# Kernel tuning notes

Measured on AMD Instinct MI355X. Metric: run time of the kernel, lower is better.

The kernel has to match this reference:

```python
import jax, jax.numpy as jnp
import numpy as np

EPS = 1e-6                                   # VN leaky-relu denominator eps
BN_SCALE = np.float32(1.0 / np.sqrt(1.0 + 1e-5))  # eval-mode BatchNorm with default stats
NEG = 0.2                                    # negative_slope


def vn_lin(x, w):
    # x: [n, c, 3, ...]; w: [c, o] -> [n, o, 3, ...]
    return jnp.einsum('nc...,co->no...', x, w)


def vn_act(p, d):
    # Vector-Neuron leaky ReLU: project p off the half-space defined by direction d.
    dot = jnp.sum(p * d, axis=2, keepdims=True)
    dsq = jnp.sum(d * d, axis=2, keepdims=True)
    corr = p - (dot / (dsq + EPS)) * d
    return NEG * p + (1.0 - NEG) * jnp.where(dot >= 0, p, corr)


def score_net(x, w_vn, wd_vn, w_h1, w_h2, b_h2, temp=1.0):
    # CorrelationNet: VNLinearLeakyReLU(3 -> 2*ks) -> norm -> 1x1 convs -> softmax
    p = vn_lin(x, w_vn) * BN_SCALE           # [N, 2ks, 3, K] (VNBatchNorm ~ scalar in eval)
    d = vn_lin(x, wd_vn)
    s = vn_act(p, d)
    s = jnp.linalg.norm(s, axis=2)           # [N, 2ks, K]
    s = jax.nn.relu(jnp.einsum('nck,co->nok', s, w_h1) * BN_SCALE)  # conv1d k=1, BN, relu
    s = jnp.einsum('nck,co->nok', s, w_h2) + b_h2[None, :, None]     # last conv with bias
    return jax.nn.softmax(s / temp, axis=1)  # [N, ks, K]


def setup_inputs() -> dict:
    key = jax.random.key(0)
    k = [jax.random.fold_in(key, i) for i in range(13)]
    N, N2, K, KS, OUT = 16000, 20000, 16, 8, 64
    half = OUT // 2
    return {
        'q_pts': jax.random.normal(k[0], (N, 3), jnp.float32),
        's_pts': jax.random.normal(k[1], (N2, 3), jnp.float32),
        's_feats': jax.random.normal(k[2], (N2, 1, 3), jnp.float32),
        'neighbor_indices': jax.random.randint(k[3], (N, K), 0, N2),
        'wb': jax.random.normal(k[4], (3, KS * half), jnp.float32) * np.float32(np.sqrt(2.0 / 3.0)),
        'w_vn': jax.random.normal(k[5], (3, 2 * KS), jnp.float32) * 0.5,
        'wd_vn': jax.random.normal(k[6], (3, 2 * KS), jnp.float32) * 0.5,
        'w_h1': jax.random.normal(k[7], (2 * KS, KS), jnp.float32) * 0.25,
        'w_h2': jax.random.normal(k[8], (KS, KS), jnp.float32) * 0.35,
        'b_h2': jnp.zeros((KS,), jnp.float32),
        'wd_relu': jax.random.normal(k[9], (half, half), jnp.float32) * 0.18,
        'w_un': jax.random.normal(k[10], (half, OUT), jnp.float32) * 0.18,
        'wd_un': jax.random.normal(k[11], (half, OUT), jnp.float32) * 0.18,
    }


def reference(q_pts, s_pts, s_feats, neighbor_indices, wb, w_vn, wd_vn,
              w_h1, w_h2, b_h2, wd_relu, w_un, wd_un):
    N, K = neighbor_indices.shape
    KS = w_h2.shape[1]
    # neighbor gather + centering: [N, K, 3] -> [N, 1, 3, K]
    pts = s_pts[neighbor_indices] - q_pts[:, None]
    pts = jnp.transpose(pts, (0, 2, 1))[:, None]
    centers = jnp.broadcast_to(jnp.mean(pts, axis=-1, keepdims=True), pts.shape)
    cross = jnp.cross(pts, centers, axis=2)
    local = jnp.concatenate([pts, centers, cross], axis=1)   # [N, 3, 3, K]
    scores = score_net(local, w_vn, wd_vn, w_h1, w_h2, b_h2)  # [N, KS, K]
    # kernel-point correlation conv
    pro = jnp.einsum('ncdk,cf->nfdk', local, wb)              # [N, KS*half, 3, K]
    pro = pro.reshape(N, KS, -1, 3, K)
    pro = jnp.sum(pro * scores[:, :, None, None, :], axis=1)  # [N, half, 3, K]
    nrm = jnp.linalg.norm(pro, axis=2, keepdims=True)
    normed = pro / jnp.maximum(nrm, 1e-12)                    # F.normalize(p=2, dim=2)
    feats = jnp.mean(normed, axis=-1)                         # [N, half, 3]
    feats = vn_act(feats, vn_lin(feats, wd_relu))             # VNLeakyReLU
    out = vn_act(vn_lin(feats, w_un) * BN_SCALE, vn_lin(feats, wd_un))  # VNLinearLeakyReLU
    return out                                                # [N, out_dim, 3]
```

## Files before the change

kernel.cpp:

```cpp
#include <hip/hip_runtime.h>
#include <math.h>

#define VN_EPS   1e-6f
#define NEG      0.2f
#define POS      0.8f

typedef float v2f __attribute__((ext_vector_type(2)));
typedef float v4f __attribute__((ext_vector_type(4)));

template <int CTRL>
__device__ __forceinline__ float dpp_add(float v) {
    int s = __builtin_amdgcn_update_dpp(0, __float_as_int(v), CTRL, 0xf, 0xf, true);
    return v + __int_as_float(s);
}
__device__ __forceinline__ float row16_allsum(float v) {
    v = dpp_add<0x128>(v);
    v = dpp_add<0x124>(v);
    v = dpp_add<0x122>(v);
    v = dpp_add<0x121>(v);
    return v;
}
__device__ __forceinline__ float row16_sum15(float v) {
    v = dpp_add<0x118>(v);
    v = dpp_add<0x114>(v);
    v = dpp_add<0x112>(v);
    v = dpp_add<0x111>(v);
    return v;
}

__device__ __forceinline__ float hsum4(v4f a) {
    return (a[0] + a[1]) + (a[2] + a[3]);
}

__global__ __launch_bounds__(64, 4) void areconv_kernel(
    const float* __restrict__ q_pts,
    const float* __restrict__ s_pts,
    const int*   __restrict__ nbr,
    const float* __restrict__ wb,
    const float* __restrict__ w_vn,
    const float* __restrict__ wd_vn,
    const float* __restrict__ w_h1,
    const float* __restrict__ w_h2,
    const float* __restrict__ b_h2,
    const float* __restrict__ wd_relu,
    const float* __restrict__ w_un,
    const float* __restrict__ wd_un,
    float* __restrict__ out,
    int N)
{
    const float BN_SCALE = 0.999994993f;

    __shared__ float featsA [4][3][36];
    __shared__ float feats2A[4][3][36];

    const int lane = threadIdx.x & 63;
    const int p    = lane >> 4;
    const int k    = lane & 15;
    int n = blockIdx.x * 4 + p;
    n = (n < N) ? n : (N - 1);

    const float qx = q_pts[n * 3 + 0];
    const float qy = q_pts[n * 3 + 1];
    const float qz = q_pts[n * 3 + 2];
    const int   id = nbr[n * 16 + k];
    const float px = s_pts[id * 3 + 0] - qx;
    const float py = s_pts[id * 3 + 1] - qy;
    const float pz = s_pts[id * 3 + 2] - qz;

    const float cx = row16_allsum(px) * 0.0625f;
    const float cy = row16_allsum(py) * 0.0625f;
    const float cz = row16_allsum(pz) * 0.0625f;

    const float rx = py * cz - pz * cy;
    const float ry = pz * cx - px * cz;
    const float rz = px * cy - py * cx;

    const float L[3][3] = {{px, py, pz}, {cx, cy, cz}, {rx, ry, rz}};

    float sn[16];
#pragma unroll
    for (int o = 0; o < 16; ++o) {
        const float wv0 = w_vn[o],  wv1 = w_vn[16 + o],  wv2 = w_vn[32 + o];
        const float wd0 = wd_vn[o], wd1 = wd_vn[16 + o], wd2 = wd_vn[32 + o];
        float pv[3], dv[3];
        float dot = 0.f, dsq = 0.f;
#pragma unroll
        for (int d = 0; d < 3; ++d) {
            const float pp = BN_SCALE * (L[0][d] * wv0 + L[1][d] * wv1 + L[2][d] * wv2);
            const float dd = L[0][d] * wd0 + L[1][d] * wd1 + L[2][d] * wd2;
            pv[d] = pp; dv[d] = dd;
            dot += pp * dd;
            dsq += dd * dd;
        }
        const float f = dot * __builtin_amdgcn_rcpf(dsq + VN_EPS);
        float acc = 0.f;
#pragma unroll
        for (int d = 0; d < 3; ++d) {
            const float corr = pv[d] - f * dv[d];
            const float sel  = (dot >= 0.f) ? pv[d] : corr;
            const float a    = NEG * pv[d] + POS * sel;
            acc += a * a;
        }
        sn[o] = __builtin_amdgcn_sqrtf(acc);
    }

    float tt[8];
#pragma unroll
    for (int op = 0; op < 4; ++op) {
        v2f t = {0.f, 0.f};
#pragma unroll
        for (int c = 0; c < 16; ++c)
            t += sn[c] * (*(const v2f*)&w_h1[c * 8 + 2 * op]);
        tt[2 * op + 0] = fmaxf(t[0] * BN_SCALE, 0.f);
        tt[2 * op + 1] = fmaxf(t[1] * BN_SCALE, 0.f);
    }

    float sc[8];
    float mx = -1e30f;
#pragma unroll
    for (int op = 0; op < 4; ++op) {
        v2f u = *(const v2f*)&b_h2[2 * op];
#pragma unroll
        for (int c = 0; c < 8; ++c)
            u += tt[c] * (*(const v2f*)&w_h2[c * 8 + 2 * op]);
        sc[2 * op + 0] = u[0];
        sc[2 * op + 1] = u[1];
        mx = fmaxf(mx, fmaxf(u[0], u[1]));
    }
    float se = 0.f;
#pragma unroll
    for (int o = 0; o < 8; ++o) { sc[o] = __expf(sc[o] - mx); se += sc[o]; }
    const float inv_se = __builtin_amdgcn_rcpf(se);
#pragma unroll
    for (int o = 0; o < 8; ++o) sc[o] *= inv_se;

#pragma unroll
    for (int grp = 0; grp < 8; ++grp) {
        const int hb = grp * 4;
        v4f W0 = sc[0] * (*(const v4f*)&wb[0 * 256 + hb]);
        v4f W1 = sc[0] * (*(const v4f*)&wb[1 * 256 + hb]);
        v4f W2 = sc[0] * (*(const v4f*)&wb[2 * 256 + hb]);
#pragma unroll
        for (int s = 1; s < 8; ++s) {
            const float sv = sc[s];
            W0 += sv * (*(const v4f*)&wb[0 * 256 + s * 32 + hb]);
            W1 += sv * (*(const v4f*)&wb[1 * 256 + s * 32 + hb]);
            W2 += sv * (*(const v4f*)&wb[2 * 256 + s * 32 + hb]);
        }
        v4f V0 = L[0][0] * W0 + L[1][0] * W1 + L[2][0] * W2;
        v4f V1 = L[0][1] * W0 + L[1][1] * W1 + L[2][1] * W2;
        v4f V2 = L[0][2] * W0 + L[1][2] * W1 + L[2][2] * W2;
        v4f vv = V0 * V0 + V1 * V1 + V2 * V2;
        v4f inn;
#pragma unroll
        for (int e = 0; e < 4; ++e)
            inn[e] = __builtin_amdgcn_rsqf(fmaxf(vv[e], 1e-24f)) * 0.0625f;
        V0 *= inn; V1 *= inn; V2 *= inn;
        v4f X0, X1, X2;
#pragma unroll
        for (int e = 0; e < 4; ++e) {
            X0[e] = row16_sum15(V0[e]);
            X1[e] = row16_sum15(V1[e]);
            X2[e] = row16_sum15(V2[e]);
        }
        if (k == 15) {
            *(v4f*)&featsA[p][0][hb] = X0;
            *(v4f*)&featsA[p][1][hb] = X1;
            *(v4f*)&featsA[p][2][hb] = X2;
        }
    }

    {
        v4f a0[2], a1[2], a2[2];
#pragma unroll
        for (int j = 0; j < 2; ++j) { a0[j] = (v4f)0.f; a1[j] = (v4f)0.f; a2[j] = (v4f)0.f; }
#pragma unroll
        for (int grp = 0; grp < 8; ++grp) {
            const int hb = grp * 4;
            const v4f f0 = *(const v4f*)&featsA[p][0][hb];
            const v4f f1 = *(const v4f*)&featsA[p][1][hb];
            const v4f f2 = *(const v4f*)&featsA[p][2][hb];
#pragma unroll
            for (int j = 0; j < 2; ++j) {
                const int o = k + 16 * j;
                const v4f w4 = { wd_relu[(hb + 0) * 32 + o], wd_relu[(hb + 1) * 32 + o],
                                 wd_relu[(hb + 2) * 32 + o], wd_relu[(hb + 3) * 32 + o] };
                a0[j] += f0 * w4;
                a1[j] += f1 * w4;
                a2[j] += f2 * w4;
            }
        }
#pragma unroll
        for (int j = 0; j < 2; ++j) {
            const int o = k + 16 * j;
            const float d0 = hsum4(a0[j]);
            const float d1 = hsum4(a1[j]);
            const float d2 = hsum4(a2[j]);
            const float p0 = featsA[p][0][o];
            const float p1 = featsA[p][1][o];
            const float p2 = featsA[p][2][o];
            const float dot = p0 * d0 + p1 * d1 + p2 * d2;
            const float dsq = d0 * d0 + d1 * d1 + d2 * d2;
            const float f   = dot * __builtin_amdgcn_rcpf(dsq + VN_EPS);
            const bool  pos = (dot >= 0.f);
            feats2A[p][0][o] = NEG * p0 + POS * (pos ? p0 : (p0 - f * d0));
            feats2A[p][1][o] = NEG * p1 + POS * (pos ? p1 : (p1 - f * d1));
            feats2A[p][2][o] = NEG * p2 + POS * (pos ? p2 : (p2 - f * d2));
        }
    }

#pragma unroll
    for (int j = 0; j < 4; ++j) {
        const int o = k + 16 * j;
        v4f au0 = (v4f)0.f, au1 = (v4f)0.f, au2 = (v4f)0.f;
        v4f av0 = (v4f)0.f, av1 = (v4f)0.f, av2 = (v4f)0.f;
#pragma unroll
        for (int grp = 0; grp < 8; ++grp) {
            const int hb = grp * 4;
            const v4f f0 = *(const v4f*)&feats2A[p][0][hb];
            const v4f f1 = *(const v4f*)&feats2A[p][1][hb];
            const v4f f2 = *(const v4f*)&feats2A[p][2][hb];
            const v4f wu = { w_un[(hb + 0) * 64 + o], w_un[(hb + 1) * 64 + o],
                             w_un[(hb + 2) * 64 + o], w_un[(hb + 3) * 64 + o] };
            const v4f wd = { wd_un[(hb + 0) * 64 + o], wd_un[(hb + 1) * 64 + o],
                             wd_un[(hb + 2) * 64 + o], wd_un[(hb + 3) * 64 + o] };
            au0 += f0 * wu; au1 += f1 * wu; au2 += f2 * wu;
            av0 += f0 * wd; av1 += f1 * wd; av2 += f2 * wd;
        }
        float u0 = hsum4(au0) * BN_SCALE;
        float u1 = hsum4(au1) * BN_SCALE;
        float u2 = hsum4(au2) * BN_SCALE;
        float v0 = hsum4(av0);
        float v1 = hsum4(av1);
        float v2 = hsum4(av2);
        const float dot = u0 * v0 + u1 * v1 + u2 * v2;
        const float dsq = v0 * v0 + v1 * v1 + v2 * v2;
        const float f   = dot * __builtin_amdgcn_rcpf(dsq + VN_EPS);
        const bool  pos = (dot >= 0.f);
        const long  base = (long)n * 192 + o * 3;
        out[base + 0] = NEG * u0 + POS * (pos ? u0 : (u0 - f * v0));
        out[base + 1] = NEG * u1 + POS * (pos ? u1 : (u1 - f * v1));
        out[base + 2] = NEG * u2 + POS * (pos ? u2 : (u2 - f * v2));
    }
}

extern "C" void kernel_launch(void* const* d_in, const int* in_sizes, int n_in,
                              void* d_out, int out_size, void* d_ws, size_t ws_size,
                              hipStream_t stream) {
    const float* q_pts   = (const float*)d_in[0];
    const float* s_pts   = (const float*)d_in[1];
    const int*   nbr     = (const int*)  d_in[3];
    const float* wb      = (const float*)d_in[4];
    const float* w_vn    = (const float*)d_in[5];
    const float* wd_vn   = (const float*)d_in[6];
    const float* w_h1    = (const float*)d_in[7];
    const float* w_h2    = (const float*)d_in[8];
    const float* b_h2    = (const float*)d_in[9];
    const float* wd_relu = (const float*)d_in[10];
    const float* w_un    = (const float*)d_in[11];
    const float* wd_un   = (const float*)d_in[12];
    float* out = (float*)d_out;

    const int N = in_sizes[0] / 3;
    const int blocks = (N + 3) / 4;
    areconv_kernel<<<blocks, 64, 0, stream>>>(
        q_pts, s_pts, nbr, wb, w_vn, wd_vn, w_h1, w_h2, b_h2,
        wd_relu, w_un, wd_un, out, N);
}
```

Baseline: 108.7 us.

## Vectorize output-channel mapping in tail VN layers and widen blocks to 256

Each lane now owns contiguous output channels (2 for the VN leaky-relu direction, 4 for the final VN linear layer). Weights load as float2/float4 vectors and each lane writes 12 contiguous output floats with three float4 stores, replacing scattered scalar loads and stores. The per-lane horizontal sums across input channels go away, and blocks grow from one wave to four waves. The cost is more register pressure from the wider accumulators, and occupancy may change under the new launch bounds.

```diff
diff --git a/kernel.cpp b/kernel.cpp
--- a/kernel.cpp
+++ b/kernel.cpp
@@ -28,11 +28,7 @@
     return v;
 }
 
-__device__ __forceinline__ float hsum4(v4f a) {
-    return (a[0] + a[1]) + (a[2] + a[3]);
-}
-
-__global__ __launch_bounds__(64, 4) void areconv_kernel(
+__global__ __launch_bounds__(256, 4) void areconv_kernel(
     const float* __restrict__ q_pts,
     const float* __restrict__ s_pts,
     const int*   __restrict__ nbr,
@@ -50,13 +46,16 @@
 {
     const float BN_SCALE = 0.999994993f;
 
-    __shared__ float featsA [4][3][36];
-    __shared__ float feats2A[4][3][36];
-
-    const int lane = threadIdx.x & 63;
+    __shared__ __align__(16) float featsA [16][3][36];
+    __shared__ __align__(16) float feats2A[16][3][36];
+
+    const int tid  = threadIdx.x;
+    const int wv   = tid >> 6;
+    const int lane = tid & 63;
     const int p    = lane >> 4;
     const int k    = lane & 15;
-    int n = blockIdx.x * 4 + p;
+    const int bp   = wv * 4 + p;
+    int n = blockIdx.x * 16 + bp;
     n = (n < N) ? n : (N - 1);
 
     const float qx = q_pts[n * 3 + 0];
@@ -164,83 +163,85 @@
             X2[e] = row16_sum15(V2[e]);
         }
         if (k == 15) {
-            *(v4f*)&featsA[p][0][hb] = X0;
-            *(v4f*)&featsA[p][1][hb] = X1;
-            *(v4f*)&featsA[p][2][hb] = X2;
+            *(v4f*)&featsA[bp][0][hb] = X0;
+            *(v4f*)&featsA[bp][1][hb] = X1;
+            *(v4f*)&featsA[bp][2][hb] = X2;
         }
     }
 
     {
-        v4f a0[2], a1[2], a2[2];
-#pragma unroll
-        for (int j = 0; j < 2; ++j) { a0[j] = (v4f)0.f; a1[j] = (v4f)0.f; a2[j] = (v4f)0.f; }
+        v2f D0 = {0.f, 0.f}, D1 = D0, D2 = D0;
 #pragma unroll
         for (int grp = 0; grp < 8; ++grp) {
             const int hb = grp * 4;
-            const v4f f0 = *(const v4f*)&featsA[p][0][hb];
-            const v4f f1 = *(const v4f*)&featsA[p][1][hb];
-            const v4f f2 = *(const v4f*)&featsA[p][2][hb];
-#pragma unroll
-            for (int j = 0; j < 2; ++j) {
-                const int o = k + 16 * j;
-                const v4f w4 = { wd_relu[(hb + 0) * 32 + o], wd_relu[(hb + 1) * 32 + o],
-                                 wd_relu[(hb + 2) * 32 + o], wd_relu[(hb + 3) * 32 + o] };
-                a0[j] += f0 * w4;
-                a1[j] += f1 * w4;
-                a2[j] += f2 * w4;
+            const v4f f0 = *(const v4f*)&featsA[bp][0][hb];
+            const v4f f1 = *(const v4f*)&featsA[bp][1][hb];
+            const v4f f2 = *(const v4f*)&featsA[bp][2][hb];
+#pragma unroll
+            for (int e = 0; e < 4; ++e) {
+                const v2f w = *(const v2f*)&wd_relu[(hb + e) * 32 + 2 * k];
+                D0 += f0[e] * w;
+                D1 += f1[e] * w;
+                D2 += f2[e] * w;
             }
         }
+        v2f R0, R1, R2;
 #pragma unroll
         for (int j = 0; j < 2; ++j) {
-            const int o = k + 16 * j;
-            const float d0 = hsum4(a0[j]);
-            const float d1 = hsum4(a1[j]);
-            const float d2 = hsum4(a2[j]);
-            const float p0 = featsA[p][0][o];
-            const float p1 = featsA[p][1][o];
-            const float p2 = featsA[p][2][o];
+            const int o = 2 * k + j;
+            const float p0 = featsA[bp][0][o];
+            const float p1 = featsA[bp][1][o];
+            const float p2 = featsA[bp][2][o];
+            const float d0 = D0[j], d1 = D1[j], d2 = D2[j];
             const float dot = p0 * d0 + p1 * d1 + p2 * d2;
             const float dsq = d0 * d0 + d1 * d1 + d2 * d2;
             const float f   = dot * __builtin_amdgcn_rcpf(dsq + VN_EPS);
             const bool  pos = (dot >= 0.f);
-            feats2A[p][0][o] = NEG * p0 + POS * (pos ? p0 : (p0 - f * d0));
-            feats2A[p][1][o] = NEG * p1 + POS * (pos ? p1 : (p1 - f * d1));
-            feats2A[p][2][o] = NEG * p2 + POS * (pos ? p2 : (p2 - f * d2));
-        }
-    }
-
-#pragma unroll
-    for (int j = 0; j < 4; ++j) {
-        const int o = k + 16 * j;
-        v4f au0 = (v4f)0.f, au1 = (v4f)0.f, au2 = (v4f)0.f;
-        v4f av0 = (v4f)0.f, av1 = (v4f)0.f, av2 = (v4f)0.f;
+            R0[j] = NEG * p0 + POS * (pos ? p0 : (p0 - f * d0));
+            R1[j] = NEG * p1 + POS * (pos ? p1 : (p1 - f * d1));
+            R2[j] = NEG * p2 + POS * (pos ? p2 : (p2 - f * d2));
+        }
+        *(v2f*)&feats2A[bp][0][2 * k] = R0;
+        *(v2f*)&feats2A[bp][1][2 * k] = R1;
+        *(v2f*)&feats2A[bp][2][2 * k] = R2;
+    }
+
+    {
+        v4f AU0 = (v4f)0.f, AU1 = AU0, AU2 = AU0;
+        v4f AV0 = AU0, AV1 = AU0, AV2 = AU0;
 #pragma unroll
         for (int grp = 0; grp < 8; ++grp) {
             const int hb = grp * 4;
-            const v4f f0 = *(const v4f*)&feats2A[p][0][hb];
-            const v4f f1 = *(const v4f*)&feats2A[p][1][hb];
-            const v4f f2 = *(const v4f*)&feats2A[p][2][hb];
-            const v4f wu = { w_un[(hb + 0) * 64 + o], w_un[(hb + 1) * 64 + o],
-                             w_un[(hb + 2) * 64 + o], w_un[(hb + 3) * 64 + o] };
-            const v4f wd = { wd_un[(hb + 0) * 64 + o], wd_un[(hb + 1) * 64 + o],
-                             wd_un[(hb + 2) * 64 + o], wd_un[(hb + 3) * 64 + o] };
-            au0 += f0 * wu; au1 += f1 * wu; au2 += f2 * wu;
-            av0 += f0 * wd; av1 += f1 * wd; av2 += f2 * wd;
-        }
-        float u0 = hsum4(au0) * BN_SCALE;
-        float u1 = hsum4(au1) * BN_SCALE;
-        float u2 = hsum4(au2) * BN_SCALE;
-        float v0 = hsum4(av0);
-        float v1 = hsum4(av1);
-        float v2 = hsum4(av2);
-        const float dot = u0 * v0 + u1 * v1 + u2 * v2;
-        const float dsq = v0 * v0 + v1 * v1 + v2 * v2;
-        const float f   = dot * __builtin_amdgcn_rcpf(dsq + VN_EPS);
-        const bool  pos = (dot >= 0.f);
-        const long  base = (long)n * 192 + o * 3;
-        out[base + 0] = NEG * u0 + POS * (pos ? u0 : (u0 - f * v0));
-        out[base + 1] = NEG * u1 + POS * (pos ? u1 : (u1 - f * v1));
-        out[base + 2] = NEG * u2 + POS * (pos ? u2 : (u2 - f * v2));
+            const v4f f0 = *(const v4f*)&feats2A[bp][0][hb];
+            const v4f f1 = *(const v4f*)&feats2A[bp][1][hb];
+            const v4f f2 = *(const v4f*)&feats2A[bp][2][hb];
+#pragma unroll
+            for (int e = 0; e < 4; ++e) {
+                const v4f wu = *(const v4f*)&w_un [(hb + e) * 64 + 4 * k];
+                const v4f wd = *(const v4f*)&wd_un[(hb + e) * 64 + 4 * k];
+                AU0 += f0[e] * wu; AU1 += f1[e] * wu; AU2 += f2[e] * wu;
+                AV0 += f0[e] * wd; AV1 += f1[e] * wd; AV2 += f2[e] * wd;
+            }
+        }
+        float O[12];
+#pragma unroll
+        for (int e = 0; e < 4; ++e) {
+            const float u0 = AU0[e] * BN_SCALE;
+            const float u1 = AU1[e] * BN_SCALE;
+            const float u2 = AU2[e] * BN_SCALE;
+            const float v0 = AV0[e], v1 = AV1[e], v2 = AV2[e];
+            const float dot = u0 * v0 + u1 * v1 + u2 * v2;
+            const float dsq = v0 * v0 + v1 * v1 + v2 * v2;
+            const float f   = dot * __builtin_amdgcn_rcpf(dsq + VN_EPS);
+            const bool  pos = (dot >= 0.f);
+            O[3 * e + 0] = NEG * u0 + POS * (pos ? u0 : (u0 - f * v0));
+            O[3 * e + 1] = NEG * u1 + POS * (pos ? u1 : (u1 - f * v1));
+            O[3 * e + 2] = NEG * u2 + POS * (pos ? u2 : (u2 - f * v2));
+        }
+        float* dst = out + (long)n * 192 + 12 * k;
+        *(v4f*)(dst + 0) = *(const v4f*)&O[0];
+        *(v4f*)(dst + 4) = *(const v4f*)&O[4];
+        *(v4f*)(dst + 8) = *(const v4f*)&O[8];
     }
 }
 
@@ -262,8 +263,8 @@
     float* out = (float*)d_out;
 
     const int N = in_sizes[0] / 3;
-    const int blocks = (N + 3) / 4;
-    areconv_kernel<<<blocks, 64, 0, stream>>>(
+    const int blocks = (N + 15) / 16;
+    areconv_kernel<<<blocks, 256, 0, stream>>>(
         q_pts, s_pts, nbr, wb, w_vn, wd_vn, w_h1, w_h2, b_h2,
         wd_relu, w_un, wd_un, out, N);
 }
```

Result: no change. 108.2 us (-0.5%).
